# Optimization experiments

Hardware: AMD Instinct MI355X
Metric: run time of the kernel (lower is better)

Reference implementation:

```python
import jax, jax.numpy as jnp
import numpy as np

EPS = 1e-12  # F.normalize clamp_min eps

def _l2norm(v, axis):
    return v / jnp.maximum(jnp.linalg.norm(v, axis=axis, keepdims=True), EPS)

def setup_inputs() -> dict:
    key = jax.random.key(0)
    k1, k2, k3, k4 = jax.random.split(key, 4)
    N, C, H, W, K = 256, 128, 31, 31, 64
    x = jax.random.normal(k1, (N, C, H, W), dtype=jnp.float32)
    conv_w = jax.random.normal(k2, (K, C), dtype=jnp.float32) * 0.1   # 1x1 conv weight, no bias (vladv2=False)
    centroids = jax.random.uniform(k3, (K, C), dtype=jnp.float32)     # torch.rand init
    atten_w = jax.random.normal(k4, (C,), dtype=jnp.float32) * 0.1    # attention 1x1 conv weight
    atten_b = jnp.zeros((1,), dtype=jnp.float32)
    return {"x": x, "conv_w": conv_w, "centroids": centroids, "atten_w": atten_w, "atten_b": atten_b}

def reference(x, conv_w, centroids, atten_w, atten_b):
    N, C, H, W = x.shape
    S = H * W  # 961
    # attention head: ReLU -> Conv2d(C,1,1) -> ReLU
    hmp = jax.nn.relu(jnp.einsum('nchw,c->nhw', jax.nn.relu(x), atten_w) + atten_b[0])
    hmp_f = hmp.reshape(N, S)                     # [N,S]
    # normalize input over channel dim
    xn = _l2norm(x, axis=1)
    x_f = xn.reshape(N, C, S)                     # [N,C,S]
    x_mul = x_f * hmp_f[:, None, :]               # [N,C,S] (hmp applied once)
    # soft assignment: 1x1 conv (no bias) on xn*hmp, softmax over clusters
    soft_assign = jax.nn.softmax(jnp.einsum('kc,ncs->nks', conv_w, x_mul), axis=1)
    # fused weighted residual aggregation (hmp applied a second time, as in source)
    w = soft_assign * hmp_f[:, None, :]           # [N,K,S]
    vlad = jnp.einsum('nks,ncs->nkc', w, x_mul) - centroids[None, :, :] * jnp.sum(w, axis=-1)[:, :, None]
    vlad = _l2norm(vlad, axis=2)                  # intra-normalize per cluster
    vlad = vlad.reshape(N, -1)
    vlad = _l2norm(vlad, axis=1)
    vlad = _l2norm(vlad, axis=1)                  # source normalizes flattened vlad twice
    return vlad
```

## Files before the change

kernel.cpp:

```cpp
#include <hip/hip_runtime.h>
#include <hip/hip_bf16.h>

#define N_ 256
#define C_ 128
#define S_ 961
#define K_ 64
#define TS 64
#define NTILE 16
#define NTHREADS 512

typedef __attribute__((ext_vector_type(4))) float f32x4;
typedef __attribute__((ext_vector_type(8))) _Float16 f16x8;
typedef __attribute__((ext_vector_type(4))) _Float16 f16x4;

#define MFMAF(a, b, c) __builtin_amdgcn_mfma_f32_16x16x32_f16((a), (b), (c), 0, 0, 0)

template <int CTRL>
static __device__ __forceinline__ float dpp_add(float v) {
    int sw = __builtin_amdgcn_update_dpp(0, __builtin_bit_cast(int, v), CTRL, 0xF, 0xF, true);
    return v + __builtin_bit_cast(float, sw);
}
static __device__ __forceinline__ float wave_sum64(float v) {
    v = dpp_add<0xB1>(v);
    v = dpp_add<0x4E>(v);
    v = dpp_add<0x141>(v);
    v = dpp_add<0x140>(v);
    v += __shfl_xor(v, 16);
    v += __shfl_xor(v, 32);
    return v;
}

__global__ __launch_bounds__(NTHREADS, 1) void vlad_mfma_kernel(
    const float* __restrict__ x,
    const float* __restrict__ conv_w,
    const float* __restrict__ cent,
    const float* __restrict__ aw,
    const float* __restrict__ ab,
    float* __restrict__ out)
{
    __shared__ union {
        _Float16 xs[2][C_][72];
        float vl[K_][130];
    } sxv;
    __shared__ _Float16 s_xT[TS][136];
    __shared__ float s_d[K_][68];
    __shared__ _Float16 s_u[K_][72];
    __shared__ float s_ared[2][8][68];
    __shared__ float s_wsum[K_], s_rs[K_];
    __shared__ float s_fin;

    const int tid = threadIdx.x;
    const int n = blockIdx.x;
    const int lane = tid & 63;
    const int w = tid >> 6;
    const int la = lane & 15;
    const int lg = lane >> 4;
    const float bias = ab[0];
    const float* xn = x + (size_t)n * (C_ * S_);

    const int cb = tid >> 4;
    const int c0 = cb * 4;
    const int s0l = (tid & 15) * 4;

    float awr[4];
    #pragma unroll
    for (int r = 0; r < 4; ++r) awr[r] = aw[c0 + r];

    const int nt1 = w & 3;
    const int mtb = (w >> 2) * 2;
    f16x8 cw[2][4];
    #pragma unroll
    for (int m2 = 0; m2 < 2; ++m2) {
        const float* p = conv_w + (la + 16 * (mtb + m2)) * C_ + 8 * lg;
        #pragma unroll
        for (int cc = 0; cc < 4; ++cc)
            #pragma unroll
            for (int i = 0; i < 8; ++i)
                cw[m2][cc][i] = (_Float16)p[32 * cc + i];
    }

    const int mtb2 = (w & 1) * 2;
    const int ctb2 = (w >> 1) * 2;
    f32x4 acc2[2][2];
    #pragma unroll
    for (int m = 0; m < 2; ++m)
        #pragma unroll
        for (int ci = 0; ci < 2; ++ci) acc2[m][ci] = (f32x4){0.f, 0.f, 0.f, 0.f};

    float wpart = 0.f;
    float pxA[4][4], pxB[4][4];

    #pragma unroll
    for (int r = 0; r < 4; ++r) {
        const float* pr = xn + (size_t)(c0 + r) * S_ + s0l;
        pxA[r][0] = pr[0]; pxA[r][1] = pr[1]; pxA[r][2] = pr[2]; pxA[r][3] = pr[3];
    }

#define GEMM2_STEP(SB)                                                          \
    {                                                                           \
        _Pragma("unroll") for (int sc = 0; sc < 2; ++sc) {                      \
            f16x8 ua[2];                                                        \
            _Pragma("unroll") for (int m = 0; m < 2; ++m)                       \
                ua[m] = *(const f16x8*)&s_u[la + 16*(mtb2+m)][8*lg + 32*sc];    \
            _Pragma("unroll") for (int ci = 0; ci < 2; ++ci) {                  \
                f16x8 xb = *(const f16x8*)&sxv.xs[SB][la + 16*(ctb2+ci)][8*lg + 32*sc]; \
                _Pragma("unroll") for (int m = 0; m < 2; ++m)                   \
                    acc2[m][ci] = MFMAF(ua[m], xb, acc2[m][ci]);                \
            }                                                                   \
        }                                                                       \
    }

#define TILE_BODY(T, PXC, PXN, BUF)                                             \
{                                                                               \
                                                          \
    if ((T) + 1 < NTILE) {                                                      \
        int gs = ((T)+1)*TS + s0l;                                              \
        _Pragma("unroll") for (int r = 0; r < 4; ++r) {                         \
            const float* pr = xn + (size_t)(c0+r)*S_ + gs;                      \
            if (gs + 3 < S_) {                                                  \
                PXN[r][0]=pr[0]; PXN[r][1]=pr[1]; PXN[r][2]=pr[2]; PXN[r][3]=pr[3]; \
            } else {                                                            \
                _Pragma("unroll") for (int j = 0; j < 4; ++j)                   \
                    PXN[r][j] = (gs + j < S_) ? pr[j] : 0.f;                    \
            }                                                                   \
        }                                                                       \
    }                                                                           \
            \
    if ((T) > 0) GEMM2_STEP((BUF)^1)                                            \
                                                   \
    {                                                                           \
        float ssqp[4], hdp[4];                                                  \
        _Pragma("unroll") for (int j = 0; j < 4; ++j) { ssqp[j]=0.f; hdp[j]=0.f; } \
        _Pragma("unroll") for (int r = 0; r < 4; ++r) {                         \
            f16x4 v;                                                            \
            _Pragma("unroll") for (int j = 0; j < 4; ++j) {                     \
                float f = PXC[r][j];                                            \
                v[j] = (_Float16)f;                                             \
                ssqp[j] += f*f;                                                 \
                hdp[j]  += fmaxf(f, 0.f)*awr[r];                                \
            }                                                                   \
            *(f16x4*)&sxv.xs[BUF][c0+r][s0l] = v;                               \
        }                                                                       \
        _Pragma("unroll") for (int j = 0; j < 4; ++j) {                         \
            int srow = s0l + j;                                                 \
            int cidx = c0 ^ (((srow >> 3) & 3) << 3);                           \
            f16x4 vT = {(_Float16)PXC[0][j], (_Float16)PXC[1][j],               \
                        (_Float16)PXC[2][j], (_Float16)PXC[3][j]};              \
            *(f16x4*)&s_xT[srow][cidx] = vT;                                    \
        }                                                                       \
        _Pragma("unroll") for (int j = 0; j < 4; ++j) {                         \
            ssqp[j] += __shfl_xor(ssqp[j], 16);                                 \
            ssqp[j] += __shfl_xor(ssqp[j], 32);                                 \
            hdp[j]  += __shfl_xor(hdp[j], 16);                                  \
            hdp[j]  += __shfl_xor(hdp[j], 32);                                  \
        }                                                                       \
        if (lg == 0) {                                                          \
            f32x4 a = {ssqp[0],ssqp[1],ssqp[2],ssqp[3]};                        \
            f32x4 b = {hdp[0],hdp[1],hdp[2],hdp[3]};                            \
            *(f32x4*)&s_ared[0][w][s0l] = a;                                    \
            *(f32x4*)&s_ared[1][w][s0l] = b;                                    \
        }                                                                       \
    }                                                                           \
    __syncthreads();                                                     \
                                                 \
    {                                                                           \
        int srow = 16*nt1 + la;                                                 \
        int swz = ((srow >> 3) & 3) << 3;                                       \
        f32x4 d0 = {0.f,0.f,0.f,0.f}, d1 = {0.f,0.f,0.f,0.f};                   \
        _Pragma("unroll") for (int cc = 0; cc < 4; ++cc) {                      \
            f16x8 b = *(const f16x8*)&s_xT[srow][(8*lg + 32*cc) ^ swz];         \
            d0 = MFMAF(cw[0][cc], b, d0);                                       \
            d1 = MFMAF(cw[1][cc], b, d1);                                       \
        }                                                                       \
        _Pragma("unroll") for (int i = 0; i < 4; ++i) {                         \
            s_d[16*mtb + 4*lg + i][16*nt1 + la]     = d0[i];                    \
            s_d[16*(mtb+1) + 4*lg + i][16*nt1 + la] = d1[i];                    \
        }                                                                       \
    }                                                                           \
    __syncthreads();                                                     \
          \
    {                                                                           \
        int j8 = lane & 7, q8 = lane >> 3;                                      \
        float ssq = s_ared[0][q8][8*w + j8];                                    \
        float hd  = s_ared[1][q8][8*w + j8];                                    \
        ssq += __shfl_xor(ssq, 8); ssq += __shfl_xor(ssq, 16); ssq += __shfl_xor(ssq, 32); \
        hd  += __shfl_xor(hd, 8);  hd  += __shfl_xor(hd, 16);  hd  += __shfl_xor(hd, 32);  \
        int sg = (T)*TS + 8*w + j8;                                             \
        float hm = (sg < S_) ? fmaxf(hd + bias, 0.f) : 0.f;                     \
        float al = hm / fmaxf(sqrtf(ssq), 1e-12f);                              \
        const float* drow = &s_d[lane][8*w];                                    \
        f32x4 dA = *(const f32x4*)drow;                                         \
        f32x4 dB = *(const f32x4*)(drow + 4);                                   \
        f16x8 u8;                                                               \
        _Pragma("unroll") for (int j = 0; j < 8; ++j) {                         \
            float alj = __shfl(al, j, 8);                                       \
            float hmj = __shfl(hm, j, 8);                                       \
            float dv = ((j < 4) ? dA[j] : dB[j-4]) * alj;                       \
            float e = __expf(dv);                                               \
            float sm = wave_sum64(e);                                           \
            float wv = e * hmj * __builtin_amdgcn_rcpf(sm);                     \
            wpart += wv;                                                        \
            u8[j] = (_Float16)(wv * alj);                                       \
        }                                                                       \
        *(f16x8*)&s_u[lane][8*w] = u8;                                          \
    }                                                                           \
    __syncthreads();                                                     \
}

    for (int tp = 0; tp < NTILE; tp += 2) {
        TILE_BODY(tp,     pxA, pxB, 0)
        TILE_BODY(tp + 1, pxB, pxA, 1)
    }
    GEMM2_STEP(1)

    s_ared[0][w][lane] = wpart;
    __syncthreads();
    if (tid < K_) {
        float v = 0.f;
        #pragma unroll
        for (int q = 0; q < 8; ++q) v += s_ared[0][q][tid];
        s_wsum[tid] = v;
    }
    __syncthreads();

    {
        #pragma unroll
        for (int m = 0; m < 2; ++m) {
            #pragma unroll
            for (int ci = 0; ci < 2; ++ci) {
                int c = la + 16 * (ctb2 + ci);
                #pragma unroll
                for (int i = 0; i < 4; ++i) {
                    int k = 16 * (mtb2 + m) + 4 * lg + i;
                    sxv.vl[k][c] = acc2[m][ci][i] - cent[k * C_ + c] * s_wsum[k];
                }
            }
        }
    }
    __syncthreads();

    {
        int k = tid >> 3;
        int q = tid & 7;
        float ssq = 0.f;
        #pragma unroll
        for (int i = 0; i < 16; ++i) {
            float v = sxv.vl[k][q * 16 + i];
            ssq += v * v;
        }
        #pragma unroll
        for (int m = 1; m < 8; m <<= 1) ssq += __shfl_xor(ssq, m);
        if (q == 0) {
            float rs = 1.0f / fmaxf(sqrtf(ssq), 1e-12f);
            s_rs[k] = rs;
            s_ared[1][0][k] = ssq * rs * rs;
        }
    }
    __syncthreads();

    if (tid < 64) {
        float v = s_ared[1][0][tid];
        #pragma unroll
        for (int m = 1; m < 64; m <<= 1) v += __shfl_xor(v, m);
        if (tid == 0) {
            float n1 = sqrtf(v);
            float sc1 = 1.0f / fmaxf(n1, 1e-12f);
            float n2 = n1 * sc1;
            float sc2 = 1.0f / fmaxf(n2, 1e-12f);
            s_fin = sc1 * sc2;
        }
    }
    __syncthreads();

    {
        float fs = s_fin;
        float* on = out + (size_t)n * (K_ * C_);
        #pragma unroll
        for (int it = 0; it < 16; ++it) {
            int idx = tid + it * NTHREADS;
            int k = idx >> 7, c = idx & 127;
            on[idx] = sxv.vl[k][c] * s_rs[k] * fs;
        }
    }
}

extern "C" void kernel_launch(void* const* d_in, const int* in_sizes, int n_in,
                              void* d_out, int out_size, void* d_ws, size_t ws_size,
                              hipStream_t stream) {
    const float* x      = (const float*)d_in[0];
    const float* conv_w = (const float*)d_in[1];
    const float* cent   = (const float*)d_in[2];
    const float* aw     = (const float*)d_in[3];
    const float* ab     = (const float*)d_in[4];
    float* outp = (float*)d_out;

    vlad_mfma_kernel<<<N_, NTHREADS, 0, stream>>>(x, conv_w, cent, aw, ab, outp);
}
```

Baseline: 61.39 us.

## Split spatial range across two blocks per sample and restructure softmax

```diff
diff --git a/kernel.cpp b/kernel.cpp
--- a/kernel.cpp
+++ b/kernel.cpp
@@ -6,7 +6,7 @@
 #define S_ 961
 #define K_ 64
 #define TS 64
-#define NTILE 16
+#define NTILE_LOC 8
 #define NTHREADS 512
 
 typedef __attribute__((ext_vector_type(4))) float f32x4;
@@ -15,42 +15,28 @@
 
 #define MFMAF(a, b, c) __builtin_amdgcn_mfma_f32_16x16x32_f16((a), (b), (c), 0, 0, 0)
 
-template <int CTRL>
-static __device__ __forceinline__ float dpp_add(float v) {
-    int sw = __builtin_amdgcn_update_dpp(0, __builtin_bit_cast(int, v), CTRL, 0xF, 0xF, true);
-    return v + __builtin_bit_cast(float, sw);
-}
-static __device__ __forceinline__ float wave_sum64(float v) {
-    v = dpp_add<0xB1>(v);
-    v = dpp_add<0x4E>(v);
-    v = dpp_add<0x141>(v);
-    v = dpp_add<0x140>(v);
-    v += __shfl_xor(v, 16);
-    v += __shfl_xor(v, 32);
-    return v;
-}
-
-__global__ __launch_bounds__(NTHREADS, 1) void vlad_mfma_kernel(
+template <bool ATOMIC>
+__global__ __launch_bounds__(NTHREADS, 4) void vlad_main(
     const float* __restrict__ x,
     const float* __restrict__ conv_w,
     const float* __restrict__ cent,
     const float* __restrict__ aw,
     const float* __restrict__ ab,
-    float* __restrict__ out)
+    float* __restrict__ out,
+    float* __restrict__ ws)
 {
-    __shared__ union {
-        _Float16 xs[2][C_][72];
-        float vl[K_][130];
-    } sxv;
+    __shared__ _Float16 s_xs[2][C_][72];
     __shared__ _Float16 s_xT[TS][136];
-    __shared__ float s_d[K_][68];
     __shared__ _Float16 s_u[K_][72];
     __shared__ float s_ared[2][8][68];
-    __shared__ float s_wsum[K_], s_rs[K_];
-    __shared__ float s_fin;
+    __shared__ float s_cs[8][68];
+    __shared__ float s_wp[8][4][8];
+    __shared__ float s_wsum[K_];
 
     const int tid = threadIdx.x;
-    const int n = blockIdx.x;
+    const int bid = blockIdx.x;
+    const int n = bid >> 1, h = bid & 1;
+    const int sbase = h * (NTILE_LOC * TS);
     const int lane = tid & 63;
     const int w = tid >> 6;
     const int la = lane & 15;
@@ -68,6 +54,7 @@
 
     const int nt1 = w & 3;
     const int mtb = (w >> 2) * 2;
+    const int sc = 16 * nt1 + la;
     f16x8 cw[2][4];
     #pragma unroll
     for (int m2 = 0; m2 < 2; ++m2) {
@@ -87,23 +74,24 @@
         #pragma unroll
         for (int ci = 0; ci < 2; ++ci) acc2[m][ci] = (f32x4){0.f, 0.f, 0.f, 0.f};
 
-    float wpart = 0.f;
+    float wp0[4] = {0.f, 0.f, 0.f, 0.f};
+    float wp1[4] = {0.f, 0.f, 0.f, 0.f};
     float pxA[4][4], pxB[4][4];
 
     #pragma unroll
     for (int r = 0; r < 4; ++r) {
-        const float* pr = xn + (size_t)(c0 + r) * S_ + s0l;
+        const float* pr = xn + (size_t)(c0 + r) * S_ + sbase + s0l;
         pxA[r][0] = pr[0]; pxA[r][1] = pr[1]; pxA[r][2] = pr[2]; pxA[r][3] = pr[3];
     }
 
 #define GEMM2_STEP(SB)                                                          \
     {                                                                           \
-        _Pragma("unroll") for (int sc = 0; sc < 2; ++sc) {                      \
+        _Pragma("unroll") for (int sc2 = 0; sc2 < 2; ++sc2) {                   \
             f16x8 ua[2];                                                        \
             _Pragma("unroll") for (int m = 0; m < 2; ++m)                       \
-                ua[m] = *(const f16x8*)&s_u[la + 16*(mtb2+m)][8*lg + 32*sc];    \
+                ua[m] = *(const f16x8*)&s_u[la + 16*(mtb2+m)][8*lg + 32*sc2];   \
             _Pragma("unroll") for (int ci = 0; ci < 2; ++ci) {                  \
-                f16x8 xb = *(const f16x8*)&sxv.xs[SB][la + 16*(ctb2+ci)][8*lg + 32*sc]; \
+                f16x8 xb = *(const f16x8*)&s_xs[SB][la + 16*(ctb2+ci)][8*lg + 32*sc2]; \
                 _Pragma("unroll") for (int m = 0; m < 2; ++m)                   \
                     acc2[m][ci] = MFMAF(ua[m], xb, acc2[m][ci]);                \
             }                                                                   \
@@ -113,8 +101,8 @@
 #define TILE_BODY(T, PXC, PXN, BUF)                                             \
 {                                                                               \
                                                           \
-    if ((T) + 1 < NTILE) {                                                      \
-        int gs = ((T)+1)*TS + s0l;                                              \
+    if ((T) + 1 < NTILE_LOC) {                                                  \
+        int gs = sbase + ((T)+1)*TS + s0l;                                      \
         _Pragma("unroll") for (int r = 0; r < 4; ++r) {                         \
             const float* pr = xn + (size_t)(c0+r)*S_ + gs;                      \
             if (gs + 3 < S_) {                                                  \
@@ -125,7 +113,7 @@
             }                                                                   \
         }                                                                       \
     }                                                                           \
-            \
+                                         \
     if ((T) > 0) GEMM2_STEP((BUF)^1)                                            \
                                                    \
     {                                                                           \
@@ -139,7 +127,7 @@
                 ssqp[j] += f*f;                                                 \
                 hdp[j]  += fmaxf(f, 0.f)*awr[r];                                \
             }                                                                   \
-            *(f16x4*)&sxv.xs[BUF][c0+r][s0l] = v;                               \
+            *(f16x4*)&s_xs[BUF][c0+r][s0l] = v;                                 \
         }                                                                       \
         _Pragma("unroll") for (int j = 0; j < 4; ++j) {                         \
             int srow = s0l + j;                                                 \
@@ -162,9 +150,10 @@
         }                                                                       \
     }                                                                           \
     __syncthreads();                                                     \
-                                                 \
+             \
+    float e0[4], e1[4], hm, al, csw;                                            \
     {                                                                           \
-        int srow = 16*nt1 + la;                                                 \
+        int srow = sc;                                                          \
         int swz = ((srow >> 3) & 3) << 3;                                       \
         f32x4 d0 = {0.f,0.f,0.f,0.f}, d1 = {0.f,0.f,0.f,0.f};                   \
         _Pragma("unroll") for (int cc = 0; cc < 4; ++cc) {                      \
@@ -172,58 +161,76 @@
             d0 = MFMAF(cw[0][cc], b, d0);                                       \
             d1 = MFMAF(cw[1][cc], b, d1);                                       \
         }                                                                       \
+        float ssq = s_ared[0][2*lg][sc] + s_ared[0][2*lg+1][sc];                \
+        float hd  = s_ared[1][2*lg][sc] + s_ared[1][2*lg+1][sc];                \
+        ssq += __shfl_xor(ssq, 16); ssq += __shfl_xor(ssq, 32);                 \
+        hd  += __shfl_xor(hd, 16);  hd  += __shfl_xor(hd, 32);                  \
+        int sg = sbase + (T)*TS + sc;                                           \
+        hm = (sg < S_) ? fmaxf(hd + bias, 0.f) : 0.f;                           \
+        al = hm / fmaxf(sqrtf(ssq), 1e-12f);                                    \
+        float cs = 0.f;                                                         \
         _Pragma("unroll") for (int i = 0; i < 4; ++i) {                         \
-            s_d[16*mtb + 4*lg + i][16*nt1 + la]     = d0[i];                    \
-            s_d[16*(mtb+1) + 4*lg + i][16*nt1 + la] = d1[i];                    \
-        }                                                                       \
+            e0[i] = __expf(d0[i] * al);                                         \
+            e1[i] = __expf(d1[i] * al);                                         \
+            cs += e0[i] + e1[i];                                                \
+        }                                                                       \
+        cs += __shfl_xor(cs, 16); cs += __shfl_xor(cs, 32);                     \
+        csw = cs;                                                               \
+        if (lg == 0) s_cs[w][sc] = cs;                                          \
     }                                                                           \
     __syncthreads();                                                     \
-          \
+                                                  \
     {                                                                           \
-        int j8 = lane & 7, q8 = lane >> 3;                                      \
-        float ssq = s_ared[0][q8][8*w + j8];                                    \
-        float hd  = s_ared[1][q8][8*w + j8];                                    \
-        ssq += __shfl_xor(ssq, 8); ssq += __shfl_xor(ssq, 16); ssq += __shfl_xor(ssq, 32); \
-        hd  += __shfl_xor(hd, 8);  hd  += __shfl_xor(hd, 16);  hd  += __shfl_xor(hd, 32);  \
-        int sg = (T)*TS + 8*w + j8;                                             \
-        float hm = (sg < S_) ? fmaxf(hd + bias, 0.f) : 0.f;                     \
-        float al = hm / fmaxf(sqrtf(ssq), 1e-12f);                              \
-        const float* drow = &s_d[lane][8*w];                                    \
-        f32x4 dA = *(const f32x4*)drow;                                         \
-        f32x4 dB = *(const f32x4*)(drow + 4);                                   \
-        f16x8 u8;                                                               \
-        _Pragma("unroll") for (int j = 0; j < 8; ++j) {                         \
-            float alj = __shfl(al, j, 8);                                       \
-            float hmj = __shfl(hm, j, 8);                                       \
-            float dv = ((j < 4) ? dA[j] : dB[j-4]) * alj;                       \
-            float e = __expf(dv);                                               \
-            float sm = wave_sum64(e);                                           \
-            float wv = e * hmj * __builtin_amdgcn_rcpf(sm);                     \
-            wpart += wv;                                                        \
-            u8[j] = (_Float16)(wv * alj);                                       \
-        }                                                                       \
-        *(f16x8*)&s_u[lane][8*w] = u8;                                          \
+        float cst = csw + s_cs[w ^ 4][sc];                                      \
+        float wl = hm * __builtin_amdgcn_rcpf(cst);                             \
+        _Pragma("unroll") for (int i = 0; i < 4; ++i) {                         \
+            float wv0 = e0[i] * wl;                                             \
+            float wv1 = e1[i] * wl;                                             \
+            wp0[i] += wv0;                                                      \
+            wp1[i] += wv1;                                                      \
+            s_u[16*mtb + 4*lg + i][sc]     = (_Float16)(wv0 * al);              \
+            s_u[16*(mtb+1) + 4*lg + i][sc] = (_Float16)(wv1 * al);              \
+        }                                                                       \
     }                                                                           \
     __syncthreads();                                                     \
 }
 
-    for (int tp = 0; tp < NTILE; tp += 2) {
+    for (int tp = 0; tp < NTILE_LOC; tp += 2) {
         TILE_BODY(tp,     pxA, pxB, 0)
         TILE_BODY(tp + 1, pxB, pxA, 1)
     }
     GEMM2_STEP(1)
 
-    s_ared[0][w][lane] = wpart;
+    {
+        #pragma unroll
+        for (int i = 0; i < 4; ++i) {
+            #pragma unroll
+            for (int m = 1; m < 16; m <<= 1) {
+                wp0[i] += __shfl_xor(wp0[i], m);
+                wp1[i] += __shfl_xor(wp1[i], m);
+            }
+        }
+        if (la == 0) {
+            #pragma unroll
+            for (int i = 0; i < 4; ++i) {
+                s_wp[w][lg][i]     = wp0[i];
+                s_wp[w][lg][4 + i] = wp1[i];
+            }
+        }
+    }
     __syncthreads();
     if (tid < K_) {
+        int k = tid;
+        int kh = k >> 5, m2 = (k >> 4) & 1, lgk = (k >> 2) & 3, ik = k & 3;
         float v = 0.f;
         #pragma unroll
-        for (int q = 0; q < 8; ++q) v += s_ared[0][q][tid];
-        s_wsum[tid] = v;
+        for (int q = 0; q < 4; ++q) v += s_wp[4 * kh + q][lgk][4 * m2 + ik];
+        s_wsum[k] = v;
     }
     __syncthreads();
 
     {
+        float* dst = ATOMIC ? out : (h ? ws : out);
         #pragma unroll
         for (int m = 0; m < 2; ++m) {
             #pragma unroll
@@ -232,38 +239,53 @@
                 #pragma unroll
                 for (int i = 0; i < 4; ++i) {
                     int k = 16 * (mtb2 + m) + 4 * lg + i;
-                    sxv.vl[k][c] = acc2[m][ci][i] - cent[k * C_ + c] * s_wsum[k];
+                    float val = acc2[m][ci][i] - cent[k * C_ + c] * s_wsum[k];
+                    size_t off = (size_t)n * (K_ * C_) + k * C_ + c;
+                    if (ATOMIC) atomicAdd(&dst[off], val);
+                    else dst[off] = val;
                 }
             }
         }
     }
+}
+
+template <bool WS>
+__global__ __launch_bounds__(256) void vlad_norm(
+    float* __restrict__ out, const float* __restrict__ ws)
+{
+    __shared__ float s_rs[K_], s_f[K_];
+    __shared__ float s_fin;
+    const int n = blockIdx.x, tid = threadIdx.x;
+    const int k = tid >> 2, q = tid & 3;
+    float* po = out + (size_t)n * (K_ * C_) + k * C_ + q * 32;
+    const float* pw = ws + (size_t)n * (K_ * C_) + k * C_ + q * 32;
+
+    float v[32];
+    float ssq = 0.f;
+    #pragma unroll
+    for (int i = 0; i < 8; ++i) {
+        f32x4 a = *(const f32x4*)&po[4 * i];
+        if (WS) {
+            f32x4 b = *(const f32x4*)&pw[4 * i];
+            a[0]+=b[0]; a[1]+=b[1]; a[2]+=b[2]; a[3]+=b[3];
+        }
+        #pragma unroll
+        for (int j = 0; j < 4; ++j) { v[4*i+j] = a[j]; ssq += a[j]*a[j]; }
+    }
+    ssq += __shfl_xor(ssq, 1);
+    ssq += __shfl_xor(ssq, 2);
+    if (q == 0) {
+        float rs = 1.0f / fmaxf(sqrtf(ssq), 1e-12f);
+        s_rs[k] = rs;
+        s_f[k] = ssq * rs * rs;
+    }
     __syncthreads();
-
-    {
-        int k = tid >> 3;
-        int q = tid & 7;
-        float ssq = 0.f;
-        #pragma unroll
-        for (int i = 0; i < 16; ++i) {
-            float v = sxv.vl[k][q * 16 + i];
-            ssq += v * v;
-        }
-        #pragma unroll
-        for (int m = 1; m < 8; m <<= 1) ssq += __shfl_xor(ssq, m);
-        if (q == 0) {
-            float rs = 1.0f / fmaxf(sqrtf(ssq), 1e-12f);
-            s_rs[k] = rs;
-            s_ared[1][0][k] = ssq * rs * rs;
-        }
-    }
-    __syncthreads();
-
     if (tid < 64) {
-        float v = s_ared[1][0][tid];
-        #pragma unroll
-        for (int m = 1; m < 64; m <<= 1) v += __shfl_xor(v, m);
+        float f = s_f[tid];
+        #pragma unroll
+        for (int m = 1; m < 64; m <<= 1) f += __shfl_xor(f, m);
         if (tid == 0) {
-            float n1 = sqrtf(v);
+            float n1 = sqrtf(f);
             float sc1 = 1.0f / fmaxf(n1, 1e-12f);
             float n2 = n1 * sc1;
             float sc2 = 1.0f / fmaxf(n2, 1e-12f);
@@ -271,16 +293,11 @@
         }
     }
     __syncthreads();
-
-    {
-        float fs = s_fin;
-        float* on = out + (size_t)n * (K_ * C_);
-        #pragma unroll
-        for (int it = 0; it < 16; ++it) {
-            int idx = tid + it * NTHREADS;
-            int k = idx >> 7, c = idx & 127;
-            on[idx] = sxv.vl[k][c] * s_rs[k] * fs;
-        }
+    float sc = s_rs[k] * s_fin;
+    #pragma unroll
+    for (int i = 0; i < 8; ++i) {
+        f32x4 a = {v[4*i]*sc, v[4*i+1]*sc, v[4*i+2]*sc, v[4*i+3]*sc};
+        *(f32x4*)&po[4 * i] = a;
     }
 }
 
@@ -293,6 +310,15 @@
     const float* aw     = (const float*)d_in[3];
     const float* ab     = (const float*)d_in[4];
     float* outp = (float*)d_out;
-
-    vlad_mfma_kernel<<<N_, NTHREADS, 0, stream>>>(x, conv_w, cent, aw, ab, outp);
+    float* wsp  = (float*)d_ws;
+
+    const size_t need = (size_t)N_ * K_ * C_ * sizeof(float);
+    if (ws_size >= need) {
+        vlad_main<false><<<2 * N_, NTHREADS, 0, stream>>>(x, conv_w, cent, aw, ab, outp, wsp);
+        vlad_norm<true><<<N_, 256, 0, stream>>>(outp, wsp);
+    } else {
+        hipMemsetAsync(d_out, 0, need, stream);
+        vlad_main<true><<<2 * N_, NTHREADS, 0, stream>>>(x, conv_w, cent, aw, ab, outp, wsp);
+        vlad_norm<false><<<N_, 256, 0, stream>>>(outp, nullptr);
+    }
 }
```

Result: slower. 91.39 us (+48.9%).
